# Kernel optimization log

Hardware: AMD Instinct MI355X
Metric: run time of the kernel (lower is better)

The kernel has to match this reference:

```python
import jax, jax.numpy as jnp
import numpy as np

EPS = 1e-5   # torch F.layer_norm default eps
TOP_K = 20   # int(3*D^2 / (2*hr*N^2 + 10*D)) for D=768, N=196, hr=1.0
NUM_EXPERTS = 200  # 10 * TOP_K


def setup_inputs() -> dict:
    key = jax.random.key(0)
    ks = jax.random.split(key, 6)
    B, N, D = 32, 196, 768
    E, H = NUM_EXPERTS, 196  # H = int(N * hidden_ratio)
    s = 0.02
    return {
        "x": jax.random.normal(ks[0], (B, N, D), jnp.float32),
        "Wr": jax.random.normal(ks[1], (E, D), jnp.float32) * s,   # router.weight
        "W1": jax.random.normal(ks[2], (E, H, N), jnp.float32) * s,  # fc1.weight per expert
        "b1": jnp.zeros((E, H), jnp.float32),
        "W2": jax.random.normal(ks[3], (E, N, H), jnp.float32) * s,  # fc2.weight per expert
        "b2": jnp.zeros((E, N), jnp.float32),
        "Wo": jax.random.normal(ks[4], (D, D), jnp.float32) * s,     # out_proj.weight
        "bo": jnp.zeros((D,), jnp.float32),
    }


def reference(x, Wr, W1, b1, W2, b2, Wo, bo):
    B, N, D = x.shape
    E = Wr.shape[0]
    K = TOP_K

    # Router: per-sample routing on token-mean features
    logits = x.mean(axis=1) @ Wr.T                      # (B, E)
    probs = jax.nn.softmax(logits, axis=-1)             # (B, E)
    w, idx = jax.lax.top_k(probs, K)                    # (B, K) sorted desc, as torch.topk
    w = w / w.sum(axis=-1, keepdims=True)               # renormalize top-k weights

    # TokenMixer operates in (B, D, N) space: layernorm over tokens (no affine),
    # then fc1 (N->H), gelu(tanh), fc2 (H->N).
    xt = jnp.swapaxes(x, 1, 2)                          # (B, D, N)
    mu = xt.mean(axis=-1, keepdims=True)
    var = xt.var(axis=-1, keepdims=True)                # population var (matches F.layer_norm)
    z = (xt - mu) * jax.lax.rsqrt(var + EPS)            # (B, D, N)

    # Gather each sample's K expert weight matrices and batch the MLPs.
    W1g, b1g = W1[idx], b1[idx]                         # (B,K,H,N), (B,K,H)
    W2g, b2g = W2[idx], b2[idx]                         # (B,K,N,H), (B,K,N)

    h = jnp.einsum('bdn,bkhn->bkdh', z, W1g) + b1g[:, :, None, :]
    a = jax.nn.gelu(h, approximate=True)                # tanh-approx GELU
    o = jnp.einsum('bkdh,bknh->bkdn', a, W2g) + b2g[:, :, None, :]

    # Weighted combine over the K selected experts, back to (B, N, D)
    mix = jnp.einsum('bk,bkdn->bnd', w, o)

    out = mix @ Wo.T + bo                               # out_proj

    # Load-balancing aux loss (top-1 assignment fraction vs mean router prob)
    top1 = jax.nn.one_hot(idx[:, 0], E, dtype=probs.dtype)   # (B, E)
    aux = E * jnp.sum(probs.mean(axis=0) * top1.mean(axis=0))
    return out, aux
```

## Files before the change

### kernel.cpp

```cpp
#include <hip/hip_runtime.h>
#include <math.h>

constexpr int B  = 32;
constexpr int N  = 196;
constexpr int D  = 768;
constexpr int E  = 200;
constexpr int TK = 20;

constexpr int NGRP = 4;
constexpr int PRB  = 14336;
constexpr int EXB  = 114688;
constexpr int LK2  = 72;

typedef __bf16 bf16x8 __attribute__((ext_vector_type(8)));
typedef __bf16 bf16x4 __attribute__((ext_vector_type(4)));
typedef float  f32x4  __attribute__((ext_vector_type(4)));
typedef long   longx2 __attribute__((ext_vector_type(2)));
typedef unsigned char uchar;

#define GLDS16(gp, lp)                                                        \
  __builtin_amdgcn_global_load_lds(                                           \
      (const __attribute__((address_space(1))) void*)(gp),                    \
      (__attribute__((address_space(3))) void*)(lp), 16, 0, 0)

#define WAITVM12  __builtin_amdgcn_s_waitcnt(0x0F7C)
#define WAITVM8   __builtin_amdgcn_s_waitcnt(0x0F78)
#define WAITVM0   __builtin_amdgcn_s_waitcnt(0x0F70)
#define WAITLGKM0 __builtin_amdgcn_s_waitcnt(0xC07F)
#define BAR       __builtin_amdgcn_s_barrier()

#define KEEP64(v) asm volatile("" : : "v"(v))

__device__ __forceinline__ float gelu_fast(float x) {
  float u = x * fmaf(x * x, 0.044715f, 1.0f);
  float e = exp2f(-2.3022084f * u);
  return x * __builtin_amdgcn_rcpf(1.0f + e);
}

__device__ __forceinline__ uchar f32_to_f8(float v) {
  return (uchar)(__builtin_amdgcn_cvt_pk_fp8_f32(v, v, 0, false) & 0xff);
}

__global__ __launch_bounds__(256) void k_ln(const float* __restrict__ x,
                                            uchar* __restrict__ zb,
                                            float* __restrict__ mu) {
  int b = blockIdx.x / 12, dt = blockIdx.x % 12;
  int d0 = dt * 64;
  int t = threadIdx.x;
  int q = t >> 6, d = t & 63;
  __shared__ float ps[256], pq[256];
  __shared__ float ms[64], rss[64];
  __shared__ alignas(16) uchar zt[64 * 264];

  for (int i = t; i < 1056; i += 256) ((uint4*)zt)[i] = (uint4){0, 0, 0, 0};

  const float* xp = x + ((size_t)b * N + q * 49) * D + d0 + d;
  float v[49];
  float s = 0.f, sq = 0.f;
  #pragma unroll
  for (int n = 0; n < 49; ++n) {
    v[n] = xp[(size_t)n * D];
    s += v[n]; sq += v[n] * v[n];
  }
  ps[t] = s; pq[t] = sq;
  __syncthreads();
  if (t < 64) {
    float S = ps[t] + ps[t + 64] + ps[t + 128] + ps[t + 192];
    float Q = pq[t] + pq[t + 64] + pq[t + 128] + pq[t + 192];
    float m = S * (1.0f / N);
    float var = Q * (1.0f / N) - m * m;
    ms[t] = m; rss[t] = rsqrtf(var + 1e-5f);
    mu[(size_t)b * D + d0 + t] = m;
  }
  __syncthreads();
  float m = ms[d], r = rss[d];
  int dsw = (d >> 1) & 3;
  #pragma unroll
  for (int n = 0; n < 49; ++n) {
    int tok = q * 49 + n;
    int qp = ((tok >> 3) & 3) ^ dsw;
    int off = d * 264 + (tok >> 6) * 64 + qp * 16 + ((tok >> 5) & 1) * 8 + (tok & 7);
    zt[off] = f32_to_f8((v[n] - m) * r);
  }
  __syncthreads();
  #pragma unroll
  for (int pair = 0; pair < 4; ++pair) {
    uint4* dst = (uint4*)(zb + (((size_t)b * 4 + pair) * 768 + d0) * 64);
    const uchar* sb = zt + (t >> 2) * 264 + pair * 64 + (t & 3) * 16;
    uint2 lo = *(const uint2*)sb;
    uint2 hi = *(const uint2*)(sb + 8);
    dst[t] = (uint4){lo.x, lo.y, hi.x, hi.y};
  }
}

__global__ __launch_bounds__(256) void k_prep(
    const float* __restrict__ W1, const float* __restrict__ W2,
    const float* __restrict__ Wo,
    uchar* __restrict__ Wf, __bf16* __restrict__ Wob,
    const float* __restrict__ mu, const float* __restrict__ Wr,
    float* __restrict__ probs, int* __restrict__ idxg,
    float* __restrict__ wg) {
  int bx = blockIdx.x;
  int t = threadIdx.x;
  __shared__ float smu[768];
  __shared__ float sp[E];
  __shared__ float smax, ssum;
  __shared__ float svals[TK];
  __shared__ int   sidx[TK];

  if (bx < 800) {
    int e = bx >> 2, mat = (bx >> 1) & 1, part = bx & 1;
    const float* src = (mat ? W2 : W1) + (size_t)e * 196 * 196;
    uchar* dst = Wf + (size_t)e * EXB + mat * 4 * PRB;
    #pragma unroll 2
    for (int it = 0; it < 14; ++it) {
      int h = part * 3584 + it * 256 + t;
      int p = h / 1792, r = h - p * 1792;
      int col = r >> 3, qp = (r >> 1) & 3, hi = r & 1;
      int ql = qp ^ ((col >> 1) & 3);
      int kst = p * 64 + hi * 32 + ql * 8;
      unsigned long out = 0ul;
      if (col < 196 && kst < 196) {
        const float* rp = src + (size_t)col * 196 + kst;
        float f0, f1, f2, f3, f4, f5, f6, f7;
        if (kst + 8 <= 196) {
          float4 v0 = *(const float4*)rp;
          float4 v1 = *(const float4*)(rp + 4);
          f0 = v0.x; f1 = v0.y; f2 = v0.z; f3 = v0.w;
          f4 = v1.x; f5 = v1.y; f6 = v1.z; f7 = v1.w;
        } else {
          f0 = rp[0]; f1 = rp[1]; f2 = rp[2]; f3 = rp[3];
          f4 = 0.f; f5 = 0.f; f6 = 0.f; f7 = 0.f;
        }
        unsigned w0 = (unsigned)__builtin_amdgcn_cvt_pk_fp8_f32(f0, f1, 0, false);
        w0 = (unsigned)__builtin_amdgcn_cvt_pk_fp8_f32(f2, f3, (int)w0, true);
        unsigned w1 = (unsigned)__builtin_amdgcn_cvt_pk_fp8_f32(f4, f5, 0, false);
        w1 = (unsigned)__builtin_amdgcn_cvt_pk_fp8_f32(f6, f7, (int)w1, true);
        out = (unsigned long)w0 | ((unsigned long)w1 << 32);
      }
      *(unsigned long*)&dst[(size_t)h * 8] = out;
    }
    return;
  }

  if (bx < 1376) {
    int i = (bx - 800) * 256 + t;
    float4 v = *(const float4*)&Wo[(size_t)i * 4];
    bf16x4 o = {(__bf16)v.x, (__bf16)v.y, (__bf16)v.z, (__bf16)v.w};
    *(bf16x4*)&Wob[(size_t)i * 4] = o;
    return;
  }

  int b = bx - 1376;
  int lane = t & 63, wave = t >> 6;
  for (int i = t; i < 768; i += 256) smu[i] = mu[(size_t)b * D + i];
  __syncthreads();
  const float4* m4 = (const float4*)smu;
  #pragma unroll 1
  for (int i = 0; i < 50; ++i) {
    int e = wave * 50 + i;
    const float4* wr4 = (const float4*)(Wr + (size_t)e * D);
    float acc = 0.f;
    #pragma unroll
    for (int j = 0; j < 3; ++j) {
      float4 w = wr4[lane + j * 64], mm = m4[lane + j * 64];
      acc = fmaf(w.x, mm.x, acc); acc = fmaf(w.y, mm.y, acc);
      acc = fmaf(w.z, mm.z, acc); acc = fmaf(w.w, mm.w, acc);
    }
    #pragma unroll
    for (int off = 32; off > 0; off >>= 1) acc += __shfl_down(acc, off);
    if (lane == 0) sp[e] = acc;
  }
  __syncthreads();
  if (t < 64) {
    float mx = -1e30f;
    for (int e = t; e < E; e += 64) mx = fmaxf(mx, sp[e]);
    #pragma unroll
    for (int off = 32; off > 0; off >>= 1) mx = fmaxf(mx, __shfl_down(mx, off));
    if (t == 0) smax = mx;
  }
  __syncthreads();
  if (t < E) sp[t] = exp2f((sp[t] - smax) * 1.44269504f);
  __syncthreads();
  if (t < 64) {
    float s = 0.f;
    for (int e = t; e < E; e += 64) s += sp[e];
    #pragma unroll
    for (int off = 32; off > 0; off >>= 1) s += __shfl_down(s, off);
    if (t == 0) ssum = s;
  }
  __syncthreads();
  if (t < E) {
    sp[t] = sp[t] / ssum;
    probs[(size_t)b * E + t] = sp[t];
  }
  __syncthreads();
  for (int k = 0; k < TK; ++k) {
    if (t < 64) {
      float bv = -1e30f; int bi = 0;
      for (int e = t; e < E; e += 64) {
        float v = sp[e];
        if (v > bv) { bv = v; bi = e; }
      }
      #pragma unroll
      for (int off = 32; off > 0; off >>= 1) {
        float ov = __shfl_down(bv, off);
        int   oi = __shfl_down(bi, off);
        if (ov > bv || (ov == bv && oi < bi)) { bv = ov; bi = oi; }
      }
      if (t == 0) {
        svals[k] = bv; sidx[k] = bi;
        sp[bi] = -2e30f;
      }
    }
    __syncthreads();
  }
  if (t == 0) {
    float s = 0.f;
    for (int k = 0; k < TK; ++k) s += svals[k];
    float inv = 1.0f / s;
    for (int k = 0; k < TK; ++k) {
      wg[b * TK + k]   = svals[k] * inv;
      idxg[b * TK + k] = sidx[k];
    }
  }
}

__global__ __launch_bounds__(256, 2) void k_expert(
    const uchar* __restrict__ zb, const uchar* __restrict__ Wf,
    const float* __restrict__ b1, const float* __restrict__ b2,
    const int* __restrict__ idxg, const float* __restrict__ wg,
    __bf16* __restrict__ mixg) {
  __shared__ alignas(16) uchar pool[75776];
  __shared__ alignas(16) __bf16 b1s[5 * 196];
  __shared__ float bsum_s[196];
  __shared__ int   eidx_s[5];
  __shared__ float w_s[5];
  uchar* zs  = pool;
  uchar* at  = pool + 16384;
  uchar* wsb = pool + 32768;
  __bf16* tb = (__bf16*)pool;

  int xw = blockIdx.x & 7, rr_ = blockIdx.x >> 3;
  int j = rr_ / 12, dt = rr_ - j * 12;
  int gid = j * 8 + xw;
  int g = gid & 3, b = gid >> 2;
  int d0 = dt * 64;

  int t = threadIdx.x;
  int lane = t & 63, wave = t >> 6;
  int quad = lane >> 4, l16 = lane & 15;
  int wrow = (wave & 1) * 32;
  int wcol = (wave >> 1) * 112;
  int qp = quad ^ ((l16 >> 1) & 3);

  if (t < 5) {
    eidx_s[t] = idxg[b * TK + g * 5 + t];
    w_s[t]    = wg[b * TK + g * 5 + t];
  }
  for (int i = t; i < 980; i += 256) {
    int kk = i / 196, col = i - kk * 196;
    int ee = idxg[b * TK + g * 5 + kk];
    b1s[i] = (__bf16)b1[ee * 196 + col];
  }
  if (t < 196) {
    float s = 0.f;
    #pragma unroll
    for (int k5 = 0; k5 < 5; ++k5) {
      int ee = idxg[b * TK + g * 5 + k5];
      s += wg[b * TK + g * 5 + k5] * b2[ee * 196 + t];
    }
    bsum_s[t] = s;
  }
  __syncthreads();

  {
    const uchar* zbase = zb + ((size_t)b * 4 * 768 + d0) * 64;
    #pragma unroll
    for (int p = 0; p < 4; ++p)
      GLDS16(zbase + (size_t)p * (768 * 64) + t * 16, zs + p * 4096 + t * 16);
  }

  int s0 = t * 16, s1 = (t + 256) * 16, s2 = (t + 512) * 16;
  int s3 = ((t & 127) + 768) * 16;

  auto issue = [&](int qn) {
    int qq = qn > 39 ? 39 : qn;
    int kk2 = qq >> 3, rem = qq & 7;
    const uchar* src = Wf + (size_t)eidx_s[kk2] * EXB + rem * PRB;
    int bi = qn & 3;
    uchar* lb = (bi == 3) ? pool : wsb + bi * PRB;
    GLDS16(src + s0, lb + s0);
    GLDS16(src + s1, lb + s1);
    GLDS16(src + s2, lb + s2);
    GLDS16(src + s3, lb + s3);
  };
  issue(0); issue(1); issue(2);

  WAITVM12;
  BAR;
  const uchar* zbase_l = zs + (wrow + l16) * 64 + qp * 16;
  longx2 zf[3][2];
  #pragma unroll
  for (int p = 0; p < 3; ++p) {
    zf[p][0] = *(const longx2*)(zbase_l + p * 4096);
    zf[p][1] = *(const longx2*)(zbase_l + p * 4096 + 1024);
  }
  long z3r0, z3r1;
  {
    longx2 zt0 = *(const longx2*)(zbase_l + 3 * 4096);
    longx2 zt1 = *(const longx2*)(zbase_l + 3 * 4096 + 1024);
    KEEP64(zt0[1]); KEEP64(zt1[1]);
    z3r0 = zt0[0]; z3r1 = zt1[0];
  }

  const uchar* abase = at + (wrow + l16) * 64 + qp * 16;

  f32x4 macc[14];
  #pragma unroll
  for (int i = 0; i < 14; ++i) macc[i] = (f32x4){0.f, 0.f, 0.f, 0.f};

  #pragma unroll 1
  for (int kk = 0; kk < 5; ++kk) {
    float wkv = w_s[kk];
    f32x4 hacc[14];
    #pragma unroll
    for (int i = 0; i < 14; ++i) hacc[i] = (f32x4){0.f, 0.f, 0.f, 0.f};

    #pragma unroll 1
    for (int p = 0; p < 3; ++p) {
      int q = kk * 8 + p;
      WAITVM8;
      BAR;
      int bi = q & 3;
      const uchar* buf = (bi == 3) ? pool : wsb + bi * PRB;
      const uchar* bb = buf + (wcol + l16) * 64 + qp * 16;
      __builtin_amdgcn_s_setprio(1);
      #pragma unroll
      for (int ct = 0; ct < 7; ++ct) {
        longx2 bf = *(const longx2*)(bb + ct * 1024);
        hacc[ct]     = __builtin_amdgcn_mfma_f32_16x16x32_fp8_fp8(bf[0], zf[p][0][0], hacc[ct], 0, 0, 0);
        hacc[ct]     = __builtin_amdgcn_mfma_f32_16x16x32_fp8_fp8(bf[1], zf[p][0][1], hacc[ct], 0, 0, 0);
        hacc[7 + ct] = __builtin_amdgcn_mfma_f32_16x16x32_fp8_fp8(bf[0], zf[p][1][0], hacc[7 + ct], 0, 0, 0);
        hacc[7 + ct] = __builtin_amdgcn_mfma_f32_16x16x32_fp8_fp8(bf[1], zf[p][1][1], hacc[7 + ct], 0, 0, 0);
      }
      __builtin_amdgcn_s_setprio(0);
      issue(q + 3);
    }
    {
      int q = kk * 8 + 3;
      WAITVM8;
      BAR;
      int bi = q & 3;
      const uchar* buf = (bi == 3) ? pool : wsb + bi * PRB;
      const uchar* bb = buf + (wcol + l16) * 64 + qp * 16;
      __builtin_amdgcn_s_setprio(1);
      #pragma unroll
      for (int ct = 0; ct < 7; ++ct) {
        longx2 bf = *(const longx2*)(bb + ct * 1024);
        KEEP64(bf[1]);
        hacc[ct]     = __builtin_amdgcn_mfma_f32_16x16x32_fp8_fp8(bf[0], z3r0, hacc[ct], 0, 0, 0);
        hacc[7 + ct] = __builtin_amdgcn_mfma_f32_16x16x32_fp8_fp8(bf[0], z3r1, hacc[7 + ct], 0, 0, 0);
      }
      __builtin_amdgcn_s_setprio(0);
      issue(q + 3);
    }

    #pragma unroll
    for (int ct = 0; ct < 7; ++ct) {
      int hb = wcol + ct * 16 + quad * 4;
      bool valid = hb < 196;
      unsigned pk0 = 0u, pk1 = 0u;
      if (valid) {
        bf16x4 b4 = *(const bf16x4*)&b1s[kk * 196 + hb];
        float bv0 = (float)b4[0], bv1 = (float)b4[1];
        float bv2 = (float)b4[2], bv3 = (float)b4[3];
        f32x4 h0 = hacc[ct], h1 = hacc[7 + ct];
        pk0 = (unsigned)__builtin_amdgcn_cvt_pk_fp8_f32(
                  gelu_fast(h0[0] + bv0) * wkv, gelu_fast(h0[1] + bv1) * wkv, 0, false);
        pk0 = (unsigned)__builtin_amdgcn_cvt_pk_fp8_f32(
                  gelu_fast(h0[2] + bv2) * wkv, gelu_fast(h0[3] + bv3) * wkv, (int)pk0, true);
        pk1 = (unsigned)__builtin_amdgcn_cvt_pk_fp8_f32(
                  gelu_fast(h1[0] + bv0) * wkv, gelu_fast(h1[1] + bv1) * wkv, 0, false);
        pk1 = (unsigned)__builtin_amdgcn_cvt_pk_fp8_f32(
                  gelu_fast(h1[2] + bv2) * wkv, gelu_fast(h1[3] + bv3) * wkv, (int)pk1, true);
      }
      int d0r = wrow + l16;
      int addr0 = (hb >> 6) * 4096 + d0r * 64 + ((((hb >> 3) & 3) ^ ((d0r >> 1) & 3)) << 4)
                + ((hb >> 5) & 1) * 8 + (quad & 1) * 4;
      *(unsigned*)&at[addr0]        = pk0;
      *(unsigned*)&at[addr0 + 1024] = pk1;
    }
    WAITLGKM0;

    #pragma unroll 1
    for (int p = 0; p < 3; ++p) {
      int q = kk * 8 + 4 + p;
      WAITVM8;
      BAR;
      int bi = q & 3;
      const uchar* buf = (bi == 3) ? pool : wsb + bi * PRB;
      const uchar* bb = buf + (wcol + l16) * 64 + qp * 16;
      longx2 a0 = *(const longx2*)(abase + p * 4096);
      longx2 a1 = *(const longx2*)(abase + p * 4096 + 1024);
      __builtin_amdgcn_s_setprio(1);
      #pragma unroll
      for (int ct = 0; ct < 7; ++ct) {
        longx2 bf = *(const longx2*)(bb + ct * 1024);
        macc[ct]     = __builtin_amdgcn_mfma_f32_16x16x32_fp8_fp8(a0[0], bf[0], macc[ct], 0, 0, 0);
        macc[ct]     = __builtin_amdgcn_mfma_f32_16x16x32_fp8_fp8(a0[1], bf[1], macc[ct], 0, 0, 0);
        macc[7 + ct] = __builtin_amdgcn_mfma_f32_16x16x32_fp8_fp8(a1[0], bf[0], macc[7 + ct], 0, 0, 0);
        macc[7 + ct] = __builtin_amdgcn_mfma_f32_16x16x32_fp8_fp8(a1[1], bf[1], macc[7 + ct], 0, 0, 0);
      }
      __builtin_amdgcn_s_setprio(0);
      issue(q + 3);
    }
    {
      int q = kk * 8 + 7;
      WAITVM8;
      BAR;
      int bi = q & 3;
      const uchar* buf = (bi == 3) ? pool : wsb + bi * PRB;
      const uchar* bb = buf + (wcol + l16) * 64 + qp * 16;
      long a0h, a1h;
      {
        longx2 at0 = *(const longx2*)(abase + 3 * 4096);
        longx2 at1 = *(const longx2*)(abase + 3 * 4096 + 1024);
        KEEP64(at0[1]); KEEP64(at1[1]);
        a0h = at0[0]; a1h = at1[0];
      }
      __builtin_amdgcn_s_setprio(1);
      #pragma unroll
      for (int ct = 0; ct < 7; ++ct) {
        longx2 bf = *(const longx2*)(bb + ct * 1024);
        KEEP64(bf[1]);
        macc[ct]     = __builtin_amdgcn_mfma_f32_16x16x32_fp8_fp8(a0h, bf[0], macc[ct], 0, 0, 0);
        macc[7 + ct] = __builtin_amdgcn_mfma_f32_16x16x32_fp8_fp8(a1h, bf[0], macc[7 + ct], 0, 0, 0);
      }
      __builtin_amdgcn_s_setprio(0);
      issue(q + 3);
    }
  }

  WAITVM0;
  BAR;
  #pragma unroll
  for (int ct = 0; ct < 7; ++ct) {
    int ncol = wcol + ct * 16 + l16;
    float bsum = (ncol < 196) ? bsum_s[ncol] : 0.f;
    #pragma unroll
    for (int rt = 0; rt < 2; ++rt) {
      f32x4 v = macc[rt * 7 + ct];
      bf16x4 o = {(__bf16)(v[0] + bsum), (__bf16)(v[1] + bsum),
                  (__bf16)(v[2] + bsum), (__bf16)(v[3] + bsum)};
      *(bf16x4*)&tb[ncol * 68 + wrow + rt * 16 + quad * 4] = o;
    }
  }
  __syncthreads();
  __bf16* mp = mixg + ((size_t)(g * B + b) * N) * D + d0;
  #pragma unroll
  for (int i = 0; i < 7; ++i) {
    int s = i * 256 + t;
    if (s < 1568) {
      int n = s >> 3, c = s & 7;
      const uint2* pa = (const uint2*)&tb[n * 68 + c * 8];
      uint2 v0 = pa[0], v1 = pa[1];
      uint4 v = {v0.x, v0.y, v1.x, v1.y};
      *(uint4*)&mp[(size_t)n * D + c * 8] = v;
    }
  }
}

__global__ __launch_bounds__(256, 3) void k_outproj(
    const __bf16* __restrict__ mixg, const __bf16* __restrict__ Wob,
    const float* __restrict__ bo, const float* __restrict__ probs,
    const int* __restrict__ idxg, float* __restrict__ out,
    float* __restrict__ out_aux) {
  __shared__ alignas(16) __bf16 As[32 * LK2];
  __shared__ alignas(16) __bf16 Bs[256 * LK2];
  const size_t GS = (size_t)B * N * D;

  int t = threadIdx.x;
  if (blockIdx.x == 0 && t < 32) {
    int top1 = idxg[t * TK];
    float s = 0.f;
    for (int bb = 0; bb < B; ++bb) s += probs[(size_t)bb * E + top1];
    #pragma unroll
    for (int off = 16; off > 0; off >>= 1) s += __shfl_down(s, off);
    if (t == 0) out_aux[0] = s * ((float)E / ((float)B * (float)B));
  }

  int m0 = (blockIdx.x % 196) * 32;
  int e0 = (blockIdx.x / 196) * 256;
  int lane = t & 63, wave = t >> 6;
  int quad = lane >> 4, l16 = lane & 15;
  int wrow = (wave & 1) * 16;
  int wcol = (wave >> 1) * 128;
  int arow = t >> 3, ach = t & 7;
  const __bf16* ap0 = mixg + (size_t)(m0 + arow) * D + ach * 8;

  f32x4 acc[8];
  #pragma unroll
  for (int i = 0; i < 8; ++i) acc[i] = (f32x4){0.f, 0.f, 0.f, 0.f};

  const uint4* wsrc = (const uint4*)Wob;
  #pragma unroll 1
  for (int c = 0; c < 12; ++c) {
    int k0 = c * 64;
    __syncthreads();
    {
      const __bf16* ap = ap0 + k0;
      bf16x8 g0 = *(const bf16x8*)(ap);
      bf16x8 g1 = *(const bf16x8*)(ap + GS);
      bf16x8 g2 = *(const bf16x8*)(ap + 2 * GS);
      bf16x8 g3 = *(const bf16x8*)(ap + 3 * GS);
      bf16x8 r;
      #pragma unroll
      for (int jj = 0; jj < 8; ++jj)
        r[jj] = (__bf16)((float)g0[jj] + (float)g1[jj] + (float)g2[jj] + (float)g3[jj]);
      *(bf16x8*)&As[arow * LK2 + ach * 8] = r;
    }
    #pragma unroll
    for (int i = 0; i < 8; ++i) {
      int p = i * 256 + t;
      int rr = p >> 3, sub = p & 7;
      uint4 v = wsrc[(((size_t)(e0 + rr)) * D + k0) / 8 + sub];
      *(uint4*)&Bs[rr * LK2 + sub * 8] = v;
    }
    __syncthreads();
    bf16x8 a0 = *(const bf16x8*)&As[(wrow + l16) * LK2 + quad * 8];
    bf16x8 a1 = *(const bf16x8*)&As[(wrow + l16) * LK2 + 32 + quad * 8];
    #pragma unroll
    for (int ct = 0; ct < 8; ++ct) {
      const __bf16* brow = &Bs[(wcol + ct * 16 + l16) * LK2];
      bf16x8 b0 = *(const bf16x8*)(brow + quad * 8);
      bf16x8 b1 = *(const bf16x8*)(brow + 32 + quad * 8);
      acc[ct] = __builtin_amdgcn_mfma_f32_16x16x32_bf16(a0, b0, acc[ct], 0, 0, 0);
      acc[ct] = __builtin_amdgcn_mfma_f32_16x16x32_bf16(a1, b1, acc[ct], 0, 0, 0);
    }
  }

  #pragma unroll
  for (int ct = 0; ct < 8; ++ct) {
    int e = e0 + wcol + ct * 16 + l16;
    float bov = bo[e];
    #pragma unroll
    for (int rx = 0; rx < 4; ++rx) {
      int m = m0 + wrow + quad * 4 + rx;
      out[(size_t)m * D + e] = acc[ct][rx] + bov;
    }
  }
}

extern "C" void kernel_launch(void* const* d_in, const int* in_sizes, int n_in,
                              void* d_out, int out_size, void* d_ws, size_t ws_size,
                              hipStream_t stream) {
  const float* x  = (const float*)d_in[0];
  const float* Wr = (const float*)d_in[1];
  const float* W1 = (const float*)d_in[2];
  const float* b1 = (const float*)d_in[3];
  const float* W2 = (const float*)d_in[4];
  const float* b2 = (const float*)d_in[5];
  const float* Wo = (const float*)d_in[6];
  const float* bo = (const float*)d_in[7];
  float* out = (float*)d_out;

  char* p = (char*)d_ws;
  auto alloc = [&](size_t bytes) {
    char* r = p;
    p += (bytes + 255) & ~(size_t)255;
    return r;
  };
  uchar*  zb   = (uchar*)alloc((size_t)B * 4 * 768 * 64);
  float*  mu   = (float*)alloc((size_t)B * D * 4);
  uchar*  Wf   = (uchar*)alloc((size_t)E * EXB);
  __bf16* Wob  = (__bf16*)alloc((size_t)D * D * 2);
  __bf16* mixg = (__bf16*)alloc((size_t)NGRP * B * N * D * 2);
  float*  probs= (float*)alloc((size_t)B * E * 4);
  int*    idxg = (int*)alloc((size_t)B * TK * 4);
  float*  wg   = (float*)alloc((size_t)B * TK * 4);

  k_ln<<<dim3(B * 12), dim3(256), 0, stream>>>(x, zb, mu);
  k_prep<<<dim3(1408), dim3(256), 0, stream>>>(W1, W2, Wo, Wf, Wob,
                                               mu, Wr, probs, idxg, wg);
  k_expert<<<dim3(1536), dim3(256), 0, stream>>>(zb, Wf, b1, b2, idxg, wg, mixg);
  k_outproj<<<dim3(588), dim3(256), 0, stream>>>(mixg, Wob, bo, probs, idxg,
                                                 out, out + (size_t)B * N * D);
}
```

Measured before the change: 334.1 us.

## Restructure expert weight streaming into paired-slab double buffering with fewer barriers

Replaces the 4-slot rolling prefetch, which waited and synchronised once per weight slab, with a scheme that loads two slabs at a time. Each pair is consumed after a full vmcnt(0) wait and a single barrier, halving the barrier count and removing per-slab buffer-index selection, and the inner loops are fully unrolled. The cost is a shallower prefetch: the wait drains all outstanding loads before the next pair is issued, so global-to-LDS latency may be less hidden. An extra LDS wait and barrier after the z fragment loads are added, presumably to guard buffer reuse.

```diff
diff --git a/kernel.cpp b/kernel.cpp
--- a/kernel.cpp
+++ b/kernel.cpp
@@ -295,9 +295,9 @@
     GLDS16(src + s2, lb + s2);
     GLDS16(src + s3, lb + s3);
   };
-  issue(0); issue(1); issue(2);
-
-  WAITVM12;
+  issue(0); issue(1);
+
+  WAITVM8;
   BAR;
   const uchar* zbase_l = zs + (wrow + l16) * 64 + qp * 16;
   longx2 zf[3][2];
@@ -313,8 +313,11 @@
     KEEP64(zt0[1]); KEEP64(zt1[1]);
     z3r0 = zt0[0]; z3r1 = zt1[0];
   }
+  WAITLGKM0;
+  BAR;
 
   const uchar* abase = at + (wrow + l16) * 64 + qp * 16;
+  const uchar* bcol  = (const uchar*)((size_t)((wcol + l16) * 64 + qp * 16));
 
   f32x4 macc[14];
   #pragma unroll
@@ -323,19 +326,18 @@
   #pragma unroll 1
   for (int kk = 0; kk < 5; ++kk) {
     float wkv = w_s[kk];
+    int q0 = kk * 8;
     f32x4 hacc[14];
     #pragma unroll
     for (int i = 0; i < 14; ++i) hacc[i] = (f32x4){0.f, 0.f, 0.f, 0.f};
 
-    #pragma unroll 1
-    for (int p = 0; p < 3; ++p) {
-      int q = kk * 8 + p;
-      WAITVM8;
-      BAR;
-      int bi = q & 3;
-      const uchar* buf = (bi == 3) ? pool : wsb + bi * PRB;
-      const uchar* bb = buf + (wcol + l16) * 64 + qp * 16;
-      __builtin_amdgcn_s_setprio(1);
+    WAITVM0;
+    BAR;
+    issue(q0 + 2); issue(q0 + 3);
+    __builtin_amdgcn_s_setprio(1);
+    #pragma unroll
+    for (int p = 0; p < 2; ++p) {
+      const uchar* bb = wsb + p * PRB + (size_t)bcol;
       #pragma unroll
       for (int ct = 0; ct < 7; ++ct) {
         longx2 bf = *(const longx2*)(bb + ct * 1024);
@@ -344,17 +346,26 @@
         hacc[7 + ct] = __builtin_amdgcn_mfma_f32_16x16x32_fp8_fp8(bf[0], zf[p][1][0], hacc[7 + ct], 0, 0, 0);
         hacc[7 + ct] = __builtin_amdgcn_mfma_f32_16x16x32_fp8_fp8(bf[1], zf[p][1][1], hacc[7 + ct], 0, 0, 0);
       }
-      __builtin_amdgcn_s_setprio(0);
-      issue(q + 3);
-    }
+    }
+    __builtin_amdgcn_s_setprio(0);
+
+    WAITVM0;
+    BAR;
+    issue(q0 + 4); issue(q0 + 5);
+    __builtin_amdgcn_s_setprio(1);
     {
-      int q = kk * 8 + 3;
-      WAITVM8;
-      BAR;
-      int bi = q & 3;
-      const uchar* buf = (bi == 3) ? pool : wsb + bi * PRB;
-      const uchar* bb = buf + (wcol + l16) * 64 + qp * 16;
-      __builtin_amdgcn_s_setprio(1);
+      const uchar* bb = wsb + 2 * PRB + (size_t)bcol;
+      #pragma unroll
+      for (int ct = 0; ct < 7; ++ct) {
+        longx2 bf = *(const longx2*)(bb + ct * 1024);
+        hacc[ct]     = __builtin_amdgcn_mfma_f32_16x16x32_fp8_fp8(bf[0], zf[2][0][0], hacc[ct], 0, 0, 0);
+        hacc[ct]     = __builtin_amdgcn_mfma_f32_16x16x32_fp8_fp8(bf[1], zf[2][0][1], hacc[ct], 0, 0, 0);
+        hacc[7 + ct] = __builtin_amdgcn_mfma_f32_16x16x32_fp8_fp8(bf[0], zf[2][1][0], hacc[7 + ct], 0, 0, 0);
+        hacc[7 + ct] = __builtin_amdgcn_mfma_f32_16x16x32_fp8_fp8(bf[1], zf[2][1][1], hacc[7 + ct], 0, 0, 0);
+      }
+    }
+    {
+      const uchar* bb = pool + (size_t)bcol;
       #pragma unroll
       for (int ct = 0; ct < 7; ++ct) {
         longx2 bf = *(const longx2*)(bb + ct * 1024);
@@ -362,9 +373,8 @@
         hacc[ct]     = __builtin_amdgcn_mfma_f32_16x16x32_fp8_fp8(bf[0], z3r0, hacc[ct], 0, 0, 0);
         hacc[7 + ct] = __builtin_amdgcn_mfma_f32_16x16x32_fp8_fp8(bf[0], z3r1, hacc[7 + ct], 0, 0, 0);
       }
-      __builtin_amdgcn_s_setprio(0);
-      issue(q + 3);
-    }
+    }
+    __builtin_amdgcn_s_setprio(0);
 
     #pragma unroll
     for (int ct = 0; ct < 7; ++ct) {
@@ -393,17 +403,15 @@
     }
     WAITLGKM0;
 
-    #pragma unroll 1
-    for (int p = 0; p < 3; ++p) {
-      int q = kk * 8 + 4 + p;
-      WAITVM8;
-      BAR;
-      int bi = q & 3;
-      const uchar* buf = (bi == 3) ? pool : wsb + bi * PRB;
-      const uchar* bb = buf + (wcol + l16) * 64 + qp * 16;
+    WAITVM0;
+    BAR;
+    issue(q0 + 6); issue(q0 + 7);
+    __builtin_amdgcn_s_setprio(1);
+    #pragma unroll
+    for (int p = 0; p < 2; ++p) {
+      const uchar* bb = wsb + p * PRB + (size_t)bcol;
       longx2 a0 = *(const longx2*)(abase + p * 4096);
       longx2 a1 = *(const longx2*)(abase + p * 4096 + 1024);
-      __builtin_amdgcn_s_setprio(1);
       #pragma unroll
       for (int ct = 0; ct < 7; ++ct) {
         longx2 bf = *(const longx2*)(bb + ct * 1024);
@@ -412,16 +420,28 @@
         macc[7 + ct] = __builtin_amdgcn_mfma_f32_16x16x32_fp8_fp8(a1[0], bf[0], macc[7 + ct], 0, 0, 0);
         macc[7 + ct] = __builtin_amdgcn_mfma_f32_16x16x32_fp8_fp8(a1[1], bf[1], macc[7 + ct], 0, 0, 0);
       }
-      __builtin_amdgcn_s_setprio(0);
-      issue(q + 3);
-    }
+    }
+    __builtin_amdgcn_s_setprio(0);
+
+    WAITVM0;
+    BAR;
+    issue(q0 + 8); issue(q0 + 9);
+    __builtin_amdgcn_s_setprio(1);
     {
-      int q = kk * 8 + 7;
-      WAITVM8;
-      BAR;
-      int bi = q & 3;
-      const uchar* buf = (bi == 3) ? pool : wsb + bi * PRB;
-      const uchar* bb = buf + (wcol + l16) * 64 + qp * 16;
+      const uchar* bb = wsb + 2 * PRB + (size_t)bcol;
+      longx2 a0 = *(const longx2*)(abase + 2 * 4096);
+      longx2 a1 = *(const longx2*)(abase + 2 * 4096 + 1024);
+      #pragma unroll
+      for (int ct = 0; ct < 7; ++ct) {
+        longx2 bf = *(const longx2*)(bb + ct * 1024);
+        macc[ct]     = __builtin_amdgcn_mfma_f32_16x16x32_fp8_fp8(a0[0], bf[0], macc[ct], 0, 0, 0);
+        macc[ct]     = __builtin_amdgcn_mfma_f32_16x16x32_fp8_fp8(a0[1], bf[1], macc[ct], 0, 0, 0);
+        macc[7 + ct] = __builtin_amdgcn_mfma_f32_16x16x32_fp8_fp8(a1[0], bf[0], macc[7 + ct], 0, 0, 0);
+        macc[7 + ct] = __builtin_amdgcn_mfma_f32_16x16x32_fp8_fp8(a1[1], bf[1], macc[7 + ct], 0, 0, 0);
+      }
+    }
+    {
+      const uchar* bb = pool + (size_t)bcol;
       long a0h, a1h;
       {
         longx2 at0 = *(const longx2*)(abase + 3 * 4096);
@@ -429,7 +449,6 @@
         KEEP64(at0[1]); KEEP64(at1[1]);
         a0h = at0[0]; a1h = at1[0];
       }
-      __builtin_amdgcn_s_setprio(1);
       #pragma unroll
       for (int ct = 0; ct < 7; ++ct) {
         longx2 bf = *(const longx2*)(bb + ct * 1024);
@@ -437,9 +456,8 @@
         macc[ct]     = __builtin_amdgcn_mfma_f32_16x16x32_fp8_fp8(a0h, bf[0], macc[ct], 0, 0, 0);
         macc[7 + ct] = __builtin_amdgcn_mfma_f32_16x16x32_fp8_fp8(a1h, bf[0], macc[7 + ct], 0, 0, 0);
       }
-      __builtin_amdgcn_s_setprio(0);
-      issue(q + 3);
-    }
+    }
+    __builtin_amdgcn_s_setprio(0);
   }
 
   WAITVM0;
```

After: 342.6 us. +2.6%, slower.
